# Performance work log

Hardware: AMD Instinct MI355X
Metric: run time of the kernel (lower is better)

## Reference

```python
import jax, jax.numpy as jnp
import numpy as np

QMAX = 255.0  # bit=8 unsigned activation range


def ste_round(x):
    # straight-through round: exact integer rounding in fwd, identity grad
    return x + jax.lax.stop_gradient(jnp.round(x) - x)


def conv3x3(x, w, stride=1):
    return jax.lax.conv_general_dilated(
        x, w, window_strides=(stride, stride), padding=((1, 1), (1, 1)),
        dimension_numbers=('NCHW', 'OIHW', 'NCHW'))


def setup_inputs() -> dict:
    key = jax.random.key(0)
    k0, k1, k2 = jax.random.split(key, 3)
    N, C, H, W = 64, 256, 28, 28
    # uint8 activations and int8 (symmetric) weights, stored as integer-valued fp32
    x = jax.random.randint(k0, (N, C, H, W), 0, 256).astype(jnp.float32)
    w1 = jax.random.randint(k1, (C, C, 3, 3), -128, 128).astype(jnp.float32)
    w2 = jax.random.randint(k2, (C, C, 3, 3), -128, 128).astype(jnp.float32)
    f = jnp.float32
    return dict(
        x=x, w1=w1, w2=w2,
        s_x=f(0.05), z_x=f(128.0),
        s_w1=f(0.01), s_conv1=f(0.08), z_conv1=f(120.0),
        s_w2=f(0.01), s_conv2=f(0.07), z_conv2=f(130.0),
        s_add=f(0.09), z_add=f(125.0))


def qconv(x_q, w_q, s_in, z_in, s_w, s_out, z_out, stride=1):
    # integer-arithmetic conv: sum((x - z_in) * w) then requantize
    acc = conv3x3(x_q - z_in, w_q, stride)
    M = s_in * s_w / s_out  # per-cluster requant multiplier (cluster 0)
    return jnp.clip(ste_round(M * acc) + z_out, 0.0, QMAX)


def qadd(a, s_a, z_a, b, s_b, z_b, s_out, z_out):
    # fused dequant of both branches + residual add + requant
    y = (s_a / s_out) * (a - z_a) + (s_b / s_out) * (b - z_b)
    return jnp.clip(ste_round(y) + z_out, 0.0, QMAX)


def reference(x, w1, w2, s_x, z_x, s_w1, s_conv1, z_conv1,
              s_w2, s_conv2, z_conv2, s_add, z_add):
    out = qconv(x, w1, s_x, z_x, s_w1, s_conv1, z_conv1)          # conv1
    out = qconv(out, w2, s_conv1, z_conv1, s_w2, s_conv2, z_conv2)  # conv2
    return qadd(x, s_x, z_x, out, s_conv2, z_conv2, s_add, z_add)   # shortcut
```

## Files before the change

kernel.cpp:

```cpp
#include <hip/hip_runtime.h>
#include <stdint.h>

#define HWP 784
#define NPOS 50176
#define PLN ((size_t)NPOS * 64)

typedef int   int4v   __attribute__((ext_vector_type(4)));
typedef int   int16v  __attribute__((ext_vector_type(16)));
typedef float float4v __attribute__((ext_vector_type(4)));
using as1_cv = const __attribute__((address_space(1))) void;
using as3_v  = __attribute__((address_space(3))) void;

__global__ __launch_bounds__(256) void k_nhwc(const float* __restrict__ x,
                                              int8_t* __restrict__ x8) {
    __shared__ int lA[256 * 15];
    __shared__ __align__(16) int lB[56 * 68];
    const int tid = threadIdx.x;
    const int P0 = blockIdx.x * 56;
    const int n = P0 / HWP;
    const int hw0 = P0 % HWP;
    const float* xb = x + (size_t)n * 256 * HWP + hw0;
#pragma unroll
    for (int k = 0; k < 14; ++k) {
        int e = tid + k * 256;
        int c = e / 14, pq = e % 14;
        float4v v = *(const float4v*)(xb + (size_t)c * HWP + pq * 4);
        int b0 = ((int)v[0] - 128) & 255;
        int b1 = ((int)v[1] - 128) & 255;
        int b2 = ((int)v[2] - 128) & 255;
        int b3 = ((int)v[3] - 128) & 255;
        lA[c * 15 + pq] = b0 | (b1 << 8) | (b2 << 16) | (b3 << 24);
    }
    __syncthreads();
#pragma unroll
    for (int k = 0; k < 4; ++k) {
        int u = tid + k * 256;
        if (u < 896) {
            int cg = u / 14, pq = u % 14;
            int d0 = lA[(cg * 4 + 0) * 15 + pq];
            int d1 = lA[(cg * 4 + 1) * 15 + pq];
            int d2 = lA[(cg * 4 + 2) * 15 + pq];
            int d3 = lA[(cg * 4 + 3) * 15 + pq];
#pragma unroll
            for (int j = 0; j < 4; ++j) {
                int sh = j * 8;
                int o = ((d0 >> sh) & 255) | (((d1 >> sh) & 255) << 8)
                      | (((d2 >> sh) & 255) << 16) | (((d3 >> sh) & 255) << 24);
                lB[(pq * 4 + j) * 68 + cg] = o;
            }
        }
    }
    __syncthreads();
#pragma unroll
    for (int k = 0; k < 4; ++k) {
        int ch = tid + k * 256;
        if (ch < 896) {
            int g = ch / 224, rem = ch % 224;
            int pos = rem >> 2, c4 = rem & 3;
            int4v val = *(const int4v*)&lB[pos * 68 + g * 16 + c4 * 4];
            *(int4v*)(x8 + (size_t)g * PLN + (size_t)(P0 + pos) * 64 + c4 * 16) = val;
        }
    }
}

__global__ __launch_bounds__(256) void k_w_prep(const float* __restrict__ w,
                                                int8_t* __restrict__ w8,
                                                int* __restrict__ wsum) {
    __shared__ int red[256];
    const int oc = blockIdx.x;
    const int t = threadIdx.x;
    const float* src = w + (size_t)oc * 2304 + (size_t)t * 9;
    const int g = oc >> 5;
    const int l = ((t >> 4) & 1) * 32 + (oc & 31);
    const int j = t & 15;
    const int s2 = (t >> 5) & 1;
    const int kb = t >> 6;
    int acc = 0;
#pragma unroll
    for (int tap = 0; tap < 9; ++tap) {
        int wv = (int)src[tap];
        acc += wv;
        int oo = ((((tap * 4 + kb) * 2 + s2) * 8 + g) * 64 + l) * 16 + j;
        w8[oo] = (int8_t)wv;
    }
    red[t] = acc;
    __syncthreads();
    for (int st = 128; st > 0; st >>= 1) {
        if (t < st) red[t] += red[t + st];
        __syncthreads();
    }
    if (t == 0) wsum[oc] = red[0];
}

template<bool FUSED>
__global__ __launch_bounds__(256, 3) void k_qconv_t(const int8_t* __restrict__ in8,
        const int8_t* __restrict__ w8, const int* __restrict__ wsum,
        const float* __restrict__ s_in_p, const float* __restrict__ s_w_p,
        const float* __restrict__ s_out_p, const float* __restrict__ z_in_p,
        const float* __restrict__ z_out_p, int8_t* __restrict__ out8,
        const int8_t* __restrict__ x8, const float* __restrict__ sxp,
        const float* __restrict__ zxp, const float* __restrict__ sap,
        const float* __restrict__ zap, float* __restrict__ outf) {
    __shared__ __align__(16) int8_t slab[47616];
    const int tid = threadIdx.x;
    const int lane = tid & 63;
    const int half = lane >> 5;
    const int wv = tid >> 6;
    const int p0 = blockIdx.x * 128;
    const int g = blockIdx.y;

    {
#pragma unroll
        for (int k = 0; k < 12; ++k) {
            int chunkid = tid + k * 256;
            if (chunkid < 2976) {
                int q = chunkid >> 4;
                int cs = chunkid & 15;
                int cg = cs ^ (q & 15);
                int qg = p0 - 29 + q;
                qg = qg < 0 ? 0 : (qg > NPOS - 1 ? NPOS - 1 : qg);
                const int8_t* src = in8 + (size_t)(cg >> 2) * PLN
                                        + (size_t)qg * 64 + (cg & 3) * 16;
                __builtin_amdgcn_global_load_lds((as1_cv*)src,
                                                 (as3_v*)&slab[chunkid * 16], 16, 0, 0);
            }
        }
    }

    const int rowpos = wv * 32 + (lane & 31);
    const int p = p0 + rowpos;
    const int hwp_ = p % HWP;
    const int ph = hwp_ / 28;
    const int pw = hwp_ % 28;

    const int zi = (int)z_in_p[0] - 128;
    const int spl = (zi & 0xff) * 0x01010101;
    int4v pad;
    pad[0] = spl; pad[1] = spl; pad[2] = spl; pad[3] = spl;

    int16v acc[2];
#pragma unroll
    for (int nt = 0; nt < 2; ++nt)
#pragma unroll
        for (int r = 0; r < 16; ++r) acc[nt][r] = 0;

    const int8_t* wlane = w8 + g * 2048 + lane * 16;
    auto loadB = [&](int u, int4v* b0, int4v* b1) {
        const int8_t* wb = wlane + (size_t)u * 16384;
        b0[0] = *(const int4v*)(wb);
        b0[1] = *(const int4v*)(wb + 1024);
        b1[0] = *(const int4v*)(wb + 8192);
        b1[1] = *(const int4v*)(wb + 9216);
    };
    int4v cb0[2], cb1[2];
    loadB(0, cb0, cb1);

    __syncthreads();

#pragma unroll 1
    for (int tap = 0; tap < 9; ++tap) {
        const int dh = tap / 3 - 1;
        const int dw = tap % 3 - 1;
        const int qrow = rowpos + dh * 28 + dw + 29;
        const bool ok = ((unsigned)(ph + dh) < 28u) & ((unsigned)(pw + dw) < 28u);
        const int sw = qrow & 15;
        const int base = qrow * 256;
#pragma unroll
        for (int kb = 0; kb < 4; ++kb) {
            const int u = tap * 4 + kb;
            int4v nb0[2], nb1[2];
            int un = u < 35 ? u + 1 : 35;
            loadB(un, nb0, nb1);
            int4v a0 = *(const int4v*)&slab[base + ((kb * 4 + half) ^ sw) * 16];
            int4v a1 = *(const int4v*)&slab[base + ((kb * 4 + 2 + half) ^ sw) * 16];
            a0 = ok ? a0 : pad;
            a1 = ok ? a1 : pad;
#pragma unroll
            for (int nt = 0; nt < 2; ++nt) {
                acc[nt] = __builtin_amdgcn_mfma_i32_32x32x32_i8(a0, cb0[nt], acc[nt], 0, 0, 0);
                acc[nt] = __builtin_amdgcn_mfma_i32_32x32x32_i8(a1, cb1[nt], acc[nt], 0, 0, 0);
            }
#pragma unroll
            for (int nt = 0; nt < 2; ++nt) { cb0[nt] = nb0[nt]; cb1[nt] = nb1[nt]; }
        }
    }

    const float Mf = s_in_p[0] * s_w_p[0] / s_out_p[0];
    const float zof = z_out_p[0];
    const int zoffi = 128 - (int)z_in_p[0];

    if (!FUSED) {
        int8_t* o8p = out8 + (size_t)g * PLN;
#pragma unroll
        for (int nt = 0; nt < 2; ++nt) {
            int oc = g * 64 + nt * 32 + (lane & 31);
            int corr = zoffi * wsum[oc];
#pragma unroll
            for (int r = 0; r < 16; ++r) {
                int row = (r & 3) + 8 * (r >> 2) + 4 * half;
                int pos = p0 + wv * 32 + row;
                float q = rintf(Mf * (float)(acc[nt][r] + corr)) + zof;
                q = fminf(fmaxf(q, 0.0f), 255.0f);
                o8p[(size_t)pos * 64 + nt * 32 + (lane & 31)] = (int8_t)((int)q - 128);
            }
        }
    } else {
        const float ra = sxp[0] / sap[0];
        const float rb = s_out_p[0] / sap[0];
        const float zx = zxp[0];
        const float z2 = z_out_p[0];
        const float za = zap[0];
        __syncthreads();
        float* tp = (float*)slab + wv * 2080;
#pragma unroll
        for (int nt = 0; nt < 2; ++nt) {
            int oc = g * 64 + nt * 32 + (lane & 31);
            int corr = zoffi * wsum[oc];
#pragma unroll
            for (int r = 0; r < 16; ++r) {
                int pl = (r & 3) + 8 * (r >> 2) + 4 * half;
                float q2 = rintf(Mf * (float)(acc[nt][r] + corr)) + zof;
                q2 = fminf(fmaxf(q2, 0.0f), 255.0f);
                tp[pl * 65 + nt * 32 + (lane & 31)] = q2;
            }
        }
        const int pl = lane & 31;
        const int hh = half;
        const int pglob = p0 + wv * 32 + pl;
        const int8_t* x8p = x8 + (size_t)g * PLN + (size_t)pglob * 64 + hh * 32;
        int4v r0 = *(const int4v*)x8p;
        int4v r1 = *(const int4v*)(x8p + 16);
        int xb[8];
        xb[0] = r0[0]; xb[1] = r0[1]; xb[2] = r0[2]; xb[3] = r0[3];
        xb[4] = r1[0]; xb[5] = r1[1]; xb[6] = r1[2]; xb[7] = r1[3];
        const int n = pglob / HWP;
        const int hwo = pglob % HWP;
        float* obase = outf + ((size_t)(n * 256 + g * 64 + hh * 32)) * HWP + hwo;
#pragma unroll
        for (int j = 0; j < 32; ++j) {
            int bv = (xb[j >> 2] >> ((j & 3) * 8)) & 255;
            int xval = (int)(int8_t)bv + 128;
            float q2 = tp[pl * 65 + hh * 32 + j];
            float y = ra * ((float)xval - zx) + rb * (q2 - z2);
            float qf = rintf(y) + za;
            qf = fminf(fmaxf(qf, 0.0f), 255.0f);
            obase[(size_t)j * HWP] = qf;
        }
    }
}

extern "C" void kernel_launch(void* const* d_in, const int* in_sizes, int n_in,
                              void* d_out, int out_size, void* d_ws, size_t ws_size,
                              hipStream_t stream) {
    (void)in_sizes; (void)n_in; (void)out_size; (void)ws_size;
    const float* x    = (const float*)d_in[0];
    const float* w1   = (const float*)d_in[1];
    const float* w2   = (const float*)d_in[2];
    const float* s_x  = (const float*)d_in[3];
    const float* z_x  = (const float*)d_in[4];
    const float* s_w1 = (const float*)d_in[5];
    const float* s_c1 = (const float*)d_in[6];
    const float* z_c1 = (const float*)d_in[7];
    const float* s_w2 = (const float*)d_in[8];
    const float* s_c2 = (const float*)d_in[9];
    const float* z_c2 = (const float*)d_in[10];
    const float* s_ad = (const float*)d_in[11];
    const float* z_ad = (const float*)d_in[12];
    float* out = (float*)d_out;

    int8_t* ws    = (int8_t*)d_ws;
    int8_t* x8    = ws;
    int8_t* o1    = ws + 12845056;
    int8_t* w8a   = ws + 25690112;
    int8_t* w8b   = ws + 26279936;
    int*    wsum1 = (int*)(ws + 26869760);
    int*    wsum2 = (int*)(ws + 26870784);

    k_nhwc<<<896, 256, 0, stream>>>(x, x8);
    k_w_prep<<<256, 256, 0, stream>>>(w1, w8a, wsum1);
    k_w_prep<<<256, 256, 0, stream>>>(w2, w8b, wsum2);
    k_qconv_t<false><<<dim3(392, 4), 256, 0, stream>>>(x8, w8a, wsum1,
        s_x, s_w1, s_c1, z_x, z_c1, o1,
        nullptr, nullptr, nullptr, nullptr, nullptr, nullptr);
    k_qconv_t<true><<<dim3(392, 4), 256, 0, stream>>>(o1, w8b, wsum2,
        s_c1, s_w2, s_c2, z_c1, z_c2, nullptr,
        x8, s_x, z_x, s_ad, z_ad, out);
}
```

Before: 215.9 us.

## Widen conv block to 128 output channels with 2x2 wave MFMA tiles

Each block now computes 128 output channels instead of 64, with each wave owning a 64x64 tile (2 M tiles by 2 N tiles), which halves the grid along channels. The input slab staged in LDS is therefore loaded half as often, and each A fragment is reused across two N tiles. The main loop is fully unrolled and double-buffers both the LDS A loads and the global B loads. Padding is handled by precomputed addresses that point into a pad region of LDS, which removes the per-load selects. The costs are roughly double the accumulator registers (64 VGPRs of acc plus buffers) at launch_bounds(256,3), a risk of spills, and fewer blocks per launch.

```diff
diff --git a/kernel.cpp b/kernel.cpp
--- a/kernel.cpp
+++ b/kernel.cpp
@@ -4,6 +4,7 @@
 #define HWP 784
 #define NPOS 50176
 #define PLN ((size_t)NPOS * 64)
+#define PAD_OFF 47616
 
 typedef int   int4v   __attribute__((ext_vector_type(4)));
 typedef int   int16v  __attribute__((ext_vector_type(16)));
@@ -101,109 +102,135 @@
         const int8_t* __restrict__ x8, const float* __restrict__ sxp,
         const float* __restrict__ zxp, const float* __restrict__ sap,
         const float* __restrict__ zap, float* __restrict__ outf) {
-    __shared__ __align__(16) int8_t slab[47616];
+    __shared__ __align__(16) int8_t slab[47872];
     const int tid = threadIdx.x;
     const int lane = tid & 63;
     const int half = lane >> 5;
     const int wv = tid >> 6;
+    const int wq = wv >> 1;
+    const int wo = wv & 1;
     const int p0 = blockIdx.x * 128;
-    const int g = blockIdx.y;
-
-    {
-#pragma unroll
-        for (int k = 0; k < 12; ++k) {
-            int chunkid = tid + k * 256;
-            if (chunkid < 2976) {
-                int q = chunkid >> 4;
-                int cs = chunkid & 15;
-                int cg = cs ^ (q & 15);
-                int qg = p0 - 29 + q;
-                qg = qg < 0 ? 0 : (qg > NPOS - 1 ? NPOS - 1 : qg);
-                const int8_t* src = in8 + (size_t)(cg >> 2) * PLN
-                                        + (size_t)qg * 64 + (cg & 3) * 16;
-                __builtin_amdgcn_global_load_lds((as1_cv*)src,
-                                                 (as3_v*)&slab[chunkid * 16], 16, 0, 0);
-            }
-        }
-    }
-
-    const int rowpos = wv * 32 + (lane & 31);
-    const int p = p0 + rowpos;
-    const int hwp_ = p % HWP;
-    const int ph = hwp_ / 28;
-    const int pw = hwp_ % 28;
+    const int gB = blockIdx.y * 128;
+
+#pragma unroll
+    for (int k = 0; k < 12; ++k) {
+        int chunkid = tid + k * 256;
+        if (chunkid < 2976) {
+            int q = chunkid >> 4;
+            int cs = chunkid & 15;
+            int cg = cs ^ (q & 15);
+            int qg = p0 - 29 + q;
+            qg = qg < 0 ? 0 : (qg > NPOS - 1 ? NPOS - 1 : qg);
+            const int8_t* src = in8 + (size_t)(cg >> 2) * PLN
+                                    + (size_t)qg * 64 + (cg & 3) * 16;
+            __builtin_amdgcn_global_load_lds((as1_cv*)src,
+                                             (as3_v*)&slab[chunkid * 16], 16, 0, 0);
+        }
+    }
 
     const int zi = (int)z_in_p[0] - 128;
     const int spl = (zi & 0xff) * 0x01010101;
-    int4v pad;
-    pad[0] = spl; pad[1] = spl; pad[2] = spl; pad[3] = spl;
-
-    int16v acc[2];
-#pragma unroll
-    for (int nt = 0; nt < 2; ++nt)
-#pragma unroll
-        for (int r = 0; r < 16; ++r) acc[nt][r] = 0;
-
-    const int8_t* wlane = w8 + g * 2048 + lane * 16;
-    auto loadB = [&](int u, int4v* b0, int4v* b1) {
-        const int8_t* wb = wlane + (size_t)u * 16384;
-        b0[0] = *(const int4v*)(wb);
-        b0[1] = *(const int4v*)(wb + 1024);
-        b1[0] = *(const int4v*)(wb + 8192);
-        b1[1] = *(const int4v*)(wb + 9216);
-    };
-    int4v cb0[2], cb1[2];
-    loadB(0, cb0, cb1);
-
-    __syncthreads();
-
-#pragma unroll 1
+    if (tid < 16) {
+        int4v pv; pv[0] = spl; pv[1] = spl; pv[2] = spl; pv[3] = spl;
+        *(int4v*)&slab[PAD_OFF + tid * 16] = pv;
+    }
+
+    int rowpos[2], ph[2], pw[2];
+#pragma unroll
+    for (int mt = 0; mt < 2; ++mt) {
+        rowpos[mt] = wq * 64 + mt * 32 + (lane & 31);
+        int p = p0 + rowpos[mt];
+        int hw = p % HWP;
+        ph[mt] = hw / 28;
+        pw[mt] = hw % 28;
+    }
+    int abz[9][2];
+#pragma unroll
     for (int tap = 0; tap < 9; ++tap) {
         const int dh = tap / 3 - 1;
         const int dw = tap % 3 - 1;
-        const int qrow = rowpos + dh * 28 + dw + 29;
-        const bool ok = ((unsigned)(ph + dh) < 28u) & ((unsigned)(pw + dw) < 28u);
-        const int sw = qrow & 15;
-        const int base = qrow * 256;
-#pragma unroll
-        for (int kb = 0; kb < 4; ++kb) {
-            const int u = tap * 4 + kb;
-            int4v nb0[2], nb1[2];
-            int un = u < 35 ? u + 1 : 35;
-            loadB(un, nb0, nb1);
-            int4v a0 = *(const int4v*)&slab[base + ((kb * 4 + half) ^ sw) * 16];
-            int4v a1 = *(const int4v*)&slab[base + ((kb * 4 + 2 + half) ^ sw) * 16];
-            a0 = ok ? a0 : pad;
-            a1 = ok ? a1 : pad;
-#pragma unroll
-            for (int nt = 0; nt < 2; ++nt) {
-                acc[nt] = __builtin_amdgcn_mfma_i32_32x32x32_i8(a0, cb0[nt], acc[nt], 0, 0, 0);
-                acc[nt] = __builtin_amdgcn_mfma_i32_32x32x32_i8(a1, cb1[nt], acc[nt], 0, 0, 0);
-            }
-#pragma unroll
-            for (int nt = 0; nt < 2; ++nt) { cb0[nt] = nb0[nt]; cb1[nt] = nb1[nt]; }
-        }
-    }
+#pragma unroll
+        for (int mt = 0; mt < 2; ++mt) {
+            int q = rowpos[mt] + dh * 28 + dw + 29;
+            bool ok = ((unsigned)(ph[mt] + dh) < 28u) & ((unsigned)(pw[mt] + dw) < 28u);
+            int base = ok ? (q << 8) : PAD_OFF;
+            abz[tap][mt] = base ^ ((q & 15) << 4) ^ (half << 4);
+        }
+    }
+
+    int16v acc[2][2];
+#pragma unroll
+    for (int mt = 0; mt < 2; ++mt)
+#pragma unroll
+        for (int nt = 0; nt < 2; ++nt)
+#pragma unroll
+            for (int r = 0; r < 16; ++r) acc[mt][nt][r] = 0;
+
+    const int gg0 = blockIdx.y * 4 + wo * 2;
+    const int8_t* wlane = w8 + gg0 * 1024 + lane * 16;
+
+    int4v areg[2][2][2];
+    int4v breg[2][2][2];
+
+#define LOADB(u, slot)                                                      \
+    {   const int8_t* wb_ = wlane + (size_t)(u) * 16384;                    \
+        breg[slot][0][0] = *(const int4v*)(wb_);                            \
+        breg[slot][1][0] = *(const int4v*)(wb_ + 1024);                     \
+        breg[slot][0][1] = *(const int4v*)(wb_ + 8192);                     \
+        breg[slot][1][1] = *(const int4v*)(wb_ + 9216); }
+#define LOADA(u, slot)                                                      \
+    {   const int tap_ = (u) >> 2, kb_ = (u) & 3;                           \
+        areg[slot][0][0] = *(const int4v*)&slab[abz[tap_][0] ^ ((kb_*4+0)<<4)]; \
+        areg[slot][0][1] = *(const int4v*)&slab[abz[tap_][0] ^ ((kb_*4+2)<<4)]; \
+        areg[slot][1][0] = *(const int4v*)&slab[abz[tap_][1] ^ ((kb_*4+0)<<4)]; \
+        areg[slot][1][1] = *(const int4v*)&slab[abz[tap_][1] ^ ((kb_*4+2)<<4)]; }
+
+    LOADB(0, 0);
+
+    __syncthreads();
+
+    LOADA(0, 0);
+#pragma unroll
+    for (int u = 0; u < 36; ++u) {
+        if (u < 35) {
+            LOADA(u + 1, (u + 1) & 1);
+            LOADB(u + 1, (u + 1) & 1);
+        }
+        const int sl = u & 1;
+#pragma unroll
+        for (int s = 0; s < 2; ++s)
+#pragma unroll
+            for (int mt = 0; mt < 2; ++mt)
+#pragma unroll
+                for (int nt = 0; nt < 2; ++nt)
+                    acc[mt][nt] = __builtin_amdgcn_mfma_i32_32x32x32_i8(
+                        areg[sl][mt][s], breg[sl][nt][s], acc[mt][nt], 0, 0, 0);
+    }
+#undef LOADA
+#undef LOADB
 
     const float Mf = s_in_p[0] * s_w_p[0] / s_out_p[0];
     const float zof = z_out_p[0];
     const int zoffi = 128 - (int)z_in_p[0];
+    const int plane = blockIdx.y * 2 + wo;
 
     if (!FUSED) {
-        int8_t* o8p = out8 + (size_t)g * PLN;
-#pragma unroll
-        for (int nt = 0; nt < 2; ++nt) {
-            int oc = g * 64 + nt * 32 + (lane & 31);
-            int corr = zoffi * wsum[oc];
-#pragma unroll
-            for (int r = 0; r < 16; ++r) {
-                int row = (r & 3) + 8 * (r >> 2) + 4 * half;
-                int pos = p0 + wv * 32 + row;
-                float q = rintf(Mf * (float)(acc[nt][r] + corr)) + zof;
-                q = fminf(fmaxf(q, 0.0f), 255.0f);
-                o8p[(size_t)pos * 64 + nt * 32 + (lane & 31)] = (int8_t)((int)q - 128);
+        int8_t* o8p = out8 + (size_t)plane * PLN;
+#pragma unroll
+        for (int mt = 0; mt < 2; ++mt)
+#pragma unroll
+            for (int nt = 0; nt < 2; ++nt) {
+                int oc = gB + wo * 64 + nt * 32 + (lane & 31);
+                int corr = zoffi * wsum[oc];
+#pragma unroll
+                for (int r = 0; r < 16; ++r) {
+                    int prow = (r & 3) + 8 * (r >> 2) + 4 * half;
+                    int pos = p0 + wq * 64 + mt * 32 + prow;
+                    float q = rintf(Mf * (float)(acc[mt][nt][r] + corr)) + zof;
+                    q = fminf(fmaxf(q, 0.0f), 255.0f);
+                    o8p[(size_t)pos * 64 + nt * 32 + (lane & 31)] = (int8_t)((int)q - 128);
+                }
             }
-        }
     } else {
         const float ra = sxp[0] / sap[0];
         const float rb = s_out_p[0] / sap[0];
@@ -212,39 +239,41 @@
         const float za = zap[0];
         __syncthreads();
         float* tp = (float*)slab + wv * 2080;
-#pragma unroll
-        for (int nt = 0; nt < 2; ++nt) {
-            int oc = g * 64 + nt * 32 + (lane & 31);
-            int corr = zoffi * wsum[oc];
-#pragma unroll
-            for (int r = 0; r < 16; ++r) {
-                int pl = (r & 3) + 8 * (r >> 2) + 4 * half;
-                float q2 = rintf(Mf * (float)(acc[nt][r] + corr)) + zof;
-                q2 = fminf(fmaxf(q2, 0.0f), 255.0f);
-                tp[pl * 65 + nt * 32 + (lane & 31)] = q2;
+        const int pl = lane & 31;
+#pragma unroll
+        for (int mt = 0; mt < 2; ++mt) {
+#pragma unroll
+            for (int nt = 0; nt < 2; ++nt) {
+                int oc = gB + wo * 64 + nt * 32 + (lane & 31);
+                int corr = zoffi * wsum[oc];
+#pragma unroll
+                for (int r = 0; r < 16; ++r) {
+                    int prow = (r & 3) + 8 * (r >> 2) + 4 * half;
+                    float q2 = rintf(Mf * (float)(acc[mt][nt][r] + corr)) + zof;
+                    q2 = fminf(fmaxf(q2, 0.0f), 255.0f);
+                    tp[prow * 65 + nt * 32 + (lane & 31)] = q2;
+                }
             }
-        }
-        const int pl = lane & 31;
-        const int hh = half;
-        const int pglob = p0 + wv * 32 + pl;
-        const int8_t* x8p = x8 + (size_t)g * PLN + (size_t)pglob * 64 + hh * 32;
-        int4v r0 = *(const int4v*)x8p;
-        int4v r1 = *(const int4v*)(x8p + 16);
-        int xb[8];
-        xb[0] = r0[0]; xb[1] = r0[1]; xb[2] = r0[2]; xb[3] = r0[3];
-        xb[4] = r1[0]; xb[5] = r1[1]; xb[6] = r1[2]; xb[7] = r1[3];
-        const int n = pglob / HWP;
-        const int hwo = pglob % HWP;
-        float* obase = outf + ((size_t)(n * 256 + g * 64 + hh * 32)) * HWP + hwo;
-#pragma unroll
-        for (int j = 0; j < 32; ++j) {
-            int bv = (xb[j >> 2] >> ((j & 3) * 8)) & 255;
-            int xval = (int)(int8_t)bv + 128;
-            float q2 = tp[pl * 65 + hh * 32 + j];
-            float y = ra * ((float)xval - zx) + rb * (q2 - z2);
-            float qf = rintf(y) + za;
-            qf = fminf(fmaxf(qf, 0.0f), 255.0f);
-            obase[(size_t)j * HWP] = qf;
+            const int pglob = p0 + wq * 64 + mt * 32 + pl;
+            const int n = pglob / HWP;
+            const int hwo = pglob % HWP;
+            const int8_t* x8p = x8 + (size_t)plane * PLN + (size_t)pglob * 64 + half * 32;
+            int4v r0 = *(const int4v*)x8p;
+            int4v r1 = *(const int4v*)(x8p + 16);
+            int xb[8];
+            xb[0] = r0[0]; xb[1] = r0[1]; xb[2] = r0[2]; xb[3] = r0[3];
+            xb[4] = r1[0]; xb[5] = r1[1]; xb[6] = r1[2]; xb[7] = r1[3];
+            float* obase = outf + ((size_t)(n * 256 + gB + wo * 64 + half * 32)) * HWP + hwo;
+#pragma unroll
+            for (int j = 0; j < 32; ++j) {
+                int bv = (xb[j >> 2] >> ((j & 3) * 8)) & 255;
+                int xval = (int)(int8_t)bv + 128;
+                float q2 = tp[pl * 65 + half * 32 + j];
+                float y = ra * ((float)xval - zx) + rb * (q2 - z2);
+                float qf = rintf(y) + za;
+                qf = fminf(fmaxf(qf, 0.0f), 255.0f);
+                obase[(size_t)j * HWP] = qf;
+            }
         }
     }
 }
@@ -279,10 +308,10 @@
     k_nhwc<<<896, 256, 0, stream>>>(x, x8);
     k_w_prep<<<256, 256, 0, stream>>>(w1, w8a, wsum1);
     k_w_prep<<<256, 256, 0, stream>>>(w2, w8b, wsum2);
-    k_qconv_t<false><<<dim3(392, 4), 256, 0, stream>>>(x8, w8a, wsum1,
+    k_qconv_t<false><<<dim3(392, 2), 256, 0, stream>>>(x8, w8a, wsum1,
         s_x, s_w1, s_c1, z_x, z_c1, o1,
         nullptr, nullptr, nullptr, nullptr, nullptr, nullptr);
-    k_qconv_t<true><<<dim3(392, 4), 256, 0, stream>>>(o1, w8b, wsum2,
+    k_qconv_t<true><<<dim3(392, 2), 256, 0, stream>>>(o1, w8b, wsum2,
         s_c1, s_w2, s_c2, z_c1, z_c2, nullptr,
         x8, s_x, z_x, s_ad, z_ad, out);
 }
```

Result: no change. 217.1 us (+0.6%).
